# Kernel optimization log

Measured on AMD Instinct MI355X. Metric: run time of the kernel, lower is better.

Reference implementation:

```python
import jax, jax.numpy as jnp
import numpy as np

DIM = 1280
HEADS = 16
HEAD_DIM = DIM // HEADS  # 80
N_CHUNKS = 8
CHUNK = 1024
TOTAL = N_CHUNKS * CHUNK  # 8192 packed tokens


def rotate_half(x):
    x1, x2 = jnp.split(x, 2, axis=-1)
    return jnp.concatenate([-x2, x1], axis=-1)


def setup_inputs() -> dict:
    key = jax.random.key(0)
    k0, k1, k2 = jax.random.split(key, 3)
    hidden_states = jax.random.normal(k0, (TOTAL, DIM), dtype=jnp.float32)
    # 2D-rope style per-token angles, duplicated halves (standard vision RoPE layout)
    inv_freq = 1.0 / (10000.0 ** (jnp.arange(0, HEAD_DIM, 2, dtype=jnp.float32) / HEAD_DIM))
    pos = jnp.arange(TOTAL, dtype=jnp.float32)
    freqs = pos[:, None] * inv_freq[None, :]            # [T, HEAD_DIM//2]
    emb = jnp.concatenate([freqs, freqs], axis=-1)      # [T, HEAD_DIM]
    cos = jnp.cos(emb)
    sin = jnp.sin(emb)
    qkv_w = jax.random.normal(k1, (3 * DIM, DIM), dtype=jnp.float32) * 0.02
    qkv_b = jnp.zeros((3 * DIM,), dtype=jnp.float32)
    proj_w = jax.random.normal(k2, (DIM, DIM), dtype=jnp.float32) * 0.02
    proj_b = jnp.zeros((DIM,), dtype=jnp.float32)
    cu_seqlens = (jnp.arange(N_CHUNKS + 1, dtype=jnp.int32) * CHUNK)
    return {"hidden_states": hidden_states, "cos": cos, "sin": sin,
            "qkv_w": qkv_w, "qkv_b": qkv_b, "proj_w": proj_w, "proj_b": proj_b,
            "cu_seqlens": cu_seqlens}


def reference(hidden_states, cos, sin, qkv_w, qkv_b, proj_w, proj_b, cu_seqlens):
    # Equal-length chunks (cu_seqlens uniform): vectorize the Python chunk loop
    # as a leading batch axis n over chunks of length L.
    n = cu_seqlens.shape[0] - 1
    total, dim = hidden_states.shape
    L = total // n
    scaling = HEAD_DIM ** -0.5

    x = hidden_states.reshape(n, L, dim)
    qkv = x @ qkv_w.T + qkv_b                              # [n, L, 3*dim]
    qkv = qkv.reshape(n, L, 3, HEADS, HEAD_DIM)
    q, k, v = qkv[:, :, 0], qkv[:, :, 1], qkv[:, :, 2]     # [n, L, H, hd]

    # inline RoPE in fp32 (matches apply_rotary_pos_emb_vision)
    c = cos.reshape(n, L, 1, HEAD_DIM).astype(jnp.float32)
    s = sin.reshape(n, L, 1, HEAD_DIM).astype(jnp.float32)
    qf = q.astype(jnp.float32)
    kf = k.astype(jnp.float32)
    q = (qf * c + rotate_half(qf) * s).astype(q.dtype)
    k = (kf * c + rotate_half(kf) * s).astype(k.dtype)

    # naive per-chunk full attention: QK^T, fp32 softmax, PV
    scores = jnp.einsum('nlhd,nmhd->nhlm', q, k) * scaling  # [n, H, L, L]
    probs = jax.nn.softmax(scores.astype(jnp.float32), axis=-1).astype(q.dtype)
    out = jnp.einsum('nhlm,nmhd->nlhd', probs, v)           # [n, L, H, hd]
    out = out.reshape(n, L, dim)
    out = out @ proj_w.T + proj_b                           # [n, L, dim]
    return out.reshape(total, dim)
```

## Files before the change

### kernel.cpp

```cpp
#include <hip/hip_runtime.h>
#include <stdint.h>

#define DIM 1280
#define HEADS 16
#define HD 80
#define TOTAL 8192
#define CHUNK 1024
#define QKVN 3840

typedef __attribute__((ext_vector_type(8))) __bf16 bf16x8;
typedef __attribute__((ext_vector_type(4))) float floatx4;

typedef __attribute__((address_space(1))) const uint32_t gu32;
typedef __attribute__((address_space(3))) uint32_t lu32;

__device__ __forceinline__ void llds16(const void* g, void* l) {
  __builtin_amdgcn_global_load_lds((gu32*)g, (lu32*)l, 16, 0, 0);
}

__device__ __forceinline__ unsigned short f2b(float f) {
  union { __bf16 b; unsigned short u; } x; x.b = (__bf16)f; return x.u;
}
__device__ __forceinline__ float b2f(unsigned short u) {
  union { __bf16 b; unsigned short u; } x; x.u = u; return (float)x.b;
}
__device__ __forceinline__ float fexp2(float x) {
#if __has_builtin(__builtin_amdgcn_exp2f)
  return __builtin_amdgcn_exp2f(x);
#else
  return __expf(x * 0.6931471805599453f);
#endif
}

#define QSCALE (0.11180339887498949f * 1.44269504088896340f)

#define KT_SH (64 * 104)
#define VT_SH (80 * 72)

__global__ void cvt_bf16(const float* __restrict__ src, unsigned short* __restrict__ dst, int n4) {
  int i = blockIdx.x * 256 + threadIdx.x;
  if (i >= n4) return;
  float4 v = reinterpret_cast<const float4*>(src)[i];
  ushort4 o;
  o.x = f2b(v.x); o.y = f2b(v.y); o.z = f2b(v.z); o.w = f2b(v.w);
  reinterpret_cast<ushort4*>(dst)[i] = o;
}


__device__ __forceinline__ void stage_a64(const unsigned short* __restrict__ G,
                                          unsigned short* ls, int wv, int lane,
                                          int row0, int kk, int hi) {
#pragma unroll
  for (int t = 0; t < 2; ++t) {
    const int stripe = t * 8 + wv;
    const int rb = ((stripe >> 3) << 7) + ((stripe & 7) << 3) + hi;
    const int r = rb + (lane >> 3);
    const int ch = (lane & 7) ^ (r & 7);
    llds16(G + (size_t)(row0 + r) * DIM + kk + (ch << 3), ls + rb * 64);
  }
}

__device__ __forceinline__ void stage_b64(const unsigned short* __restrict__ G,
                                          unsigned short* ls, int wv, int lane,
                                          int row0, int kk, int hi) {
#pragma unroll
  for (int t = 0; t < 2; ++t) {
    const int stripe = t * 8 + wv;
    const int rb = ((stripe >> 2) << 6) + ((stripe & 3) << 3) + hi;
    const int r = rb + (lane >> 3);
    const int ch = (lane & 7) ^ (r & 7);
    llds16(G + (size_t)(row0 + r) * DIM + kk + (ch << 3), ls + rb * 64);
  }
}

__device__ __forceinline__ bf16x8 frg(const unsigned short* ls, int r, int cx) {
  return *reinterpret_cast<const bf16x8*>(ls + r * 64 + (cx << 3));
}

#define MFMA_BF16 __builtin_amdgcn_mfma_f32_16x16x32_bf16
#define LGKM0() asm volatile("s_waitcnt lgkmcnt(0)" ::: "memory")
#define BARR()  asm volatile("s_barrier" ::: "memory")

template<int MODE>
__launch_bounds__(512, 2)
__global__ void gemm8(const unsigned short* __restrict__ A,
                      const unsigned short* __restrict__ B,
                      const float* __restrict__ bias,
                      unsigned short* __restrict__ qo,
                      unsigned short* __restrict__ ko,
                      unsigned short* __restrict__ vo,
                      float* __restrict__ fo) {
  __shared__ __attribute__((aligned(16))) unsigned short lsA[2][256 * 64];
  __shared__ __attribute__((aligned(16))) unsigned short lsB[2][256 * 64];
  const int m0 = blockIdx.x * 256;
  const int n0 = blockIdx.y * 256;
  const int tid = threadIdx.x;
  const int wv = tid >> 6, lane = tid & 63;
  const int wr = wv >> 2, wc = wv & 3;
  const int q4 = lane >> 4, l15 = lane & 15;
  const int sx = l15 & 7;
  const int cx0 = q4 ^ sx;
  const int cx1 = (4 + q4) ^ sx;

  stage_a64(A, &lsA[0][0], wv, lane, m0, 0, 0);
  stage_b64(B, &lsB[0][0], wv, lane, n0, 0, 0);
  stage_b64(B, &lsB[0][0], wv, lane, n0, 0, 32);
  stage_a64(A, &lsA[0][0], wv, lane, m0, 0, 64);
  stage_b64(B, &lsB[1][0], wv, lane, n0, 64, 0);
  stage_a64(A, &lsA[1][0], wv, lane, m0, 64, 0);
  stage_b64(B, &lsB[1][0], wv, lane, n0, 64, 32);

  floatx4 acc[8][4];
#pragma unroll
  for (int i = 0; i < 8; ++i)
#pragma unroll
    for (int j = 0; j < 4; ++j)
      acc[i][j] = (floatx4){0.f, 0.f, 0.f, 0.f};

  asm volatile("s_waitcnt vmcnt(6)" ::: "memory");
  BARR();

  const int rA = wr * 128 + l15;
  const int rB = wc * 64 + l15;

  bf16x8 ArLo[4][2], ArHi[4][2], Blo[2][2], Bhi[2][2];

#pragma unroll 2
  for (int kt = 0; kt < 20; ++kt) {
    const unsigned short* la = &lsA[kt & 1][0];
    const unsigned short* lb = &lsB[kt & 1][0];
    unsigned short* aN = &lsA[(kt & 1) ^ 1][0];
    unsigned short* aC = &lsA[kt & 1][0];
    unsigned short* bC = &lsB[kt & 1][0];
    const bool st1 = (kt + 1 < 20);
    const bool st2 = (kt + 2 < 20);

    if (kt > 0) {
#pragma unroll
      for (int m = 0; m < 4; ++m)
#pragma unroll
        for (int n = 0; n < 2; ++n) {
          acc[m + 4][n] = MFMA_BF16(ArHi[m][0], Blo[n][0], acc[m + 4][n], 0, 0, 0);
          acc[m + 4][n] = MFMA_BF16(ArHi[m][1], Blo[n][1], acc[m + 4][n], 0, 0, 0);
        }
    }
#pragma unroll
    for (int m = 0; m < 4; ++m) {
      ArLo[m][0] = frg(la, rA + m * 16, cx0);
      ArLo[m][1] = frg(la, rA + m * 16, cx1);
    }
#pragma unroll
    for (int n = 0; n < 2; ++n) {
      Blo[n][0] = frg(lb, rB + n * 16, cx0);
      Blo[n][1] = frg(lb, rB + n * 16, cx1);
    }
    if (st1) stage_a64(A, aN, wv, lane, m0, (kt + 1) * 64, 64);
    LGKM0();
    BARR();

#pragma unroll
    for (int m = 0; m < 4; ++m)
#pragma unroll
      for (int n = 0; n < 2; ++n) {
        acc[m][n] = MFMA_BF16(ArLo[m][0], Blo[n][0], acc[m][n], 0, 0, 0);
        acc[m][n] = MFMA_BF16(ArLo[m][1], Blo[n][1], acc[m][n], 0, 0, 0);
      }
#pragma unroll
    for (int n = 0; n < 2; ++n) {
      Bhi[n][0] = frg(lb, rB + (n + 2) * 16, cx0);
      Bhi[n][1] = frg(lb, rB + (n + 2) * 16, cx1);
    }
    if (st2) stage_b64(B, bC, wv, lane, n0, (kt + 2) * 64, 0);
    LGKM0();
    BARR();

#pragma unroll
    for (int m = 0; m < 4; ++m)
#pragma unroll
      for (int n = 0; n < 2; ++n) {
        acc[m][n + 2] = MFMA_BF16(ArLo[m][0], Bhi[n][0], acc[m][n + 2], 0, 0, 0);
        acc[m][n + 2] = MFMA_BF16(ArLo[m][1], Bhi[n][1], acc[m][n + 2], 0, 0, 0);
      }
#pragma unroll
    for (int m = 0; m < 4; ++m) {
      ArHi[m][0] = frg(la, rA + (m + 4) * 16, cx0);
      ArHi[m][1] = frg(la, rA + (m + 4) * 16, cx1);
    }
    if (st2) stage_a64(A, aC, wv, lane, m0, (kt + 2) * 64, 0);
    LGKM0();
    BARR();

#pragma unroll
    for (int m = 0; m < 4; ++m)
#pragma unroll
      for (int n = 0; n < 2; ++n) {
        acc[m + 4][n + 2] = MFMA_BF16(ArHi[m][0], Bhi[n][0], acc[m + 4][n + 2], 0, 0, 0);
        acc[m + 4][n + 2] = MFMA_BF16(ArHi[m][1], Bhi[n][1], acc[m + 4][n + 2], 0, 0, 0);
      }
    if (st2) stage_b64(B, bC, wv, lane, n0, (kt + 2) * 64, 32);
    if (st2)      asm volatile("s_waitcnt vmcnt(6)" ::: "memory");
    else if (st1) asm volatile("s_waitcnt vmcnt(0)" ::: "memory");
    BARR();
  }

#pragma unroll
  for (int m = 0; m < 4; ++m)
#pragma unroll
    for (int n = 0; n < 2; ++n) {
      acc[m + 4][n] = MFMA_BF16(ArHi[m][0], Blo[n][0], acc[m + 4][n], 0, 0, 0);
      acc[m + 4][n] = MFMA_BF16(ArHi[m][1], Blo[n][1], acc[m + 4][n], 0, 0, 0);
    }

  if (MODE == 0) {
    if (blockIdx.y >= 10) {
      unsigned short* scr = (wv < 4) ? (&lsA[0][0] + wv * 8192)
                                     : (&lsB[0][0] + (wv - 4) * 8192);
      const int base_c = n0 - 2 * DIM + wc * 64;
#pragma unroll
      for (int n = 0; n < 4; ++n) {
        const int cloc = n * 16 + l15;
        const float bn = bias[2 * DIM + base_c + cloc];
        const int swz = (cloc & 7) << 4;
#pragma unroll
        for (int m = 0; m < 8; ++m) {
          const int rloc = m * 16 + q4 * 4;
          ushort4 w;
          w.x = f2b(acc[m][n][0] + bn);
          w.y = f2b(acc[m][n][1] + bn);
          w.z = f2b(acc[m][n][2] + bn);
          w.w = f2b(acc[m][n][3] + bn);
          *reinterpret_cast<ushort4*>(scr + cloc * 128 + (rloc ^ swz)) = w;
        }
      }
#pragma unroll
      for (int jtc = 0; jtc < 2; ++jtc) {
        const int rowg = m0 + wr * 128 + jtc * 64;
        const int chn = rowg >> 10, jtn = (rowg >> 6) & 15;
#pragma unroll
        for (int cb = 0; cb < 16; ++cb) {
          const int col = cb * 4 + q4;
          const int c = base_c + col;
          const int h = c / 80;
          const int d = c - h * 80;
          const int rloc = jtc * 64 + l15 * 4;
          const ushort4 w = *reinterpret_cast<const ushort4*>(
              scr + col * 128 + (rloc ^ ((col & 7) << 4)));
          *reinterpret_cast<ushort4*>(
              vo + (size_t)((chn * 16 + h) * 16 + jtn) * VT_SH + d * 72 + l15 * 4) = w;
        }
      }
      return;
    }
    unsigned short* os;
    int nloc = n0;
    if (blockIdx.y < 5) { os = qo; }
    else                { os = ko; nloc = n0 - DIM; }
#pragma unroll
    for (int n = 0; n < 4; ++n) {
      const int cg = wc * 64 + n * 16 + l15;
      const float bn = bias[n0 + cg];
#pragma unroll
      for (int m = 0; m < 8; ++m) {
#pragma unroll
        for (int r = 0; r < 4; ++r) {
          const int row = m0 + wr * 128 + m * 16 + q4 * 4 + r;
          os[(size_t)row * DIM + nloc + cg] = f2b(acc[m][n][r] + bn);
        }
      }
    }
    return;
  }
#pragma unroll
  for (int n = 0; n < 4; ++n) {
    const int cg = wc * 64 + n * 16 + l15;
    const float bn = bias[n0 + cg];
#pragma unroll
    for (int m = 0; m < 8; ++m) {
#pragma unroll
      for (int r = 0; r < 4; ++r) {
        const int row = m0 + wr * 128 + m * 16 + q4 * 4 + r;
        fo[(size_t)row * DIM + n0 + cg] = acc[m][n][r] + bn;
      }
    }
  }
}

__global__ void prep_k(const unsigned short* __restrict__ kbuf,
                       const float* __restrict__ cp, const float* __restrict__ sp,
                       unsigned short* __restrict__ kimg) {
  const int m = blockIdx.x, tid = threadIdx.x;
  const int ch = m >> 10, rl = m & 1023;
  const int jt = rl >> 6, rr = rl & 63;

  if (tid < 160) {
    const int h = tid / 10, j = tid - h * 10;
    const int d0 = 4 * j;
    const float4 c4 = *reinterpret_cast<const float4*>(cp + (size_t)m * HD + d0);
    const float4 s4 = *reinterpret_cast<const float4*>(sp + (size_t)m * HD + d0);
    const ushort4 lo = *reinterpret_cast<const ushort4*>(kbuf + (size_t)m * DIM + h * HD + d0);
    const ushort4 hi = *reinterpret_cast<const ushort4*>(kbuf + (size_t)m * DIM + h * HD + d0 + 40);
    ushort4 o1, o2;
    o1.x = f2b(b2f(lo.x) * c4.x - b2f(hi.x) * s4.x);
    o1.y = f2b(b2f(lo.y) * c4.y - b2f(hi.y) * s4.y);
    o1.z = f2b(b2f(lo.z) * c4.z - b2f(hi.z) * s4.z);
    o1.w = f2b(b2f(lo.w) * c4.w - b2f(hi.w) * s4.w);
    o2.x = f2b(b2f(hi.x) * c4.x + b2f(lo.x) * s4.x);
    o2.y = f2b(b2f(hi.y) * c4.y + b2f(lo.y) * s4.y);
    o2.z = f2b(b2f(hi.z) * c4.z + b2f(lo.z) * s4.z);
    o2.w = f2b(b2f(hi.w) * c4.w + b2f(lo.w) * s4.w);
    const size_t ob = ((size_t)((ch * 16 + h) * 16 + jt) * KT_SH) + rr * 104;
    *reinterpret_cast<ushort4*>(kimg + ob + d0) = o1;
    *reinterpret_cast<ushort4*>(kimg + ob + d0 + 40) = o2;
  } else {
    const int t = tid - 160;
    const int h = t / 6, qi = t - h * 6;
    const size_t ob = ((size_t)((ch * 16 + h) * 16 + jt) * KT_SH) + rr * 104;
    *reinterpret_cast<ushort4*>(kimg + ob + 80 + 4 * qi) = (ushort4){0, 0, 0, 0};
  }
}

__launch_bounds__(256, 2)
__global__ void attn_k(const unsigned short* __restrict__ qbuf,
                       const unsigned short* __restrict__ kimg,
                       const unsigned short* __restrict__ vimg,
                       const float* __restrict__ cp, const float* __restrict__ sp,
                       unsigned short* __restrict__ ob) {
  __shared__ __attribute__((aligned(16))) unsigned short lsK[2][KT_SH];
  __shared__ __attribute__((aligned(16))) unsigned short lsV[2][VT_SH];
  __shared__ __attribute__((aligned(16))) unsigned short lsP[128 * 72];

  const int bx = blockIdx.x;
  const int qt = bx & 7, h = (bx >> 3) & 15, ch = bx >> 7;
  const int tid = threadIdx.x, wv = tid >> 6, lane = tid & 63;
  const int q4 = lane >> 4, l15 = lane & 15;
  const int qrow_loc = qt * 128 + wv * 32;

  bf16x8 aq[2][3];
#pragma unroll
  for (int mt = 0; mt < 2; ++mt) {
    const int m_row = ch * 1024 + qrow_loc + mt * 16 + l15;
    const unsigned short* qr = qbuf + (size_t)m_row * DIM + h * HD;
    const float* cr = cp + (size_t)m_row * HD;
    const float* sr = sp + (size_t)m_row * HD;
#pragma unroll
    for (int ks = 0; ks < 3; ++ks) {
      const int d0 = ks * 32 + q4 * 8;
      union { ushort4 u4[2]; bf16x8 v; } out;
      if (d0 < 80) {
        const bool hi = (d0 >= 40);
        const int pd = hi ? d0 - 40 : d0 + 40;
        const float sg = hi ? 1.0f : -1.0f;
        const ushort4 xa = *reinterpret_cast<const ushort4*>(qr + d0);
        const ushort4 xc = *reinterpret_cast<const ushort4*>(qr + d0 + 4);
        const ushort4 pa = *reinterpret_cast<const ushort4*>(qr + pd);
        const ushort4 pc = *reinterpret_cast<const ushort4*>(qr + pd + 4);
        const float4 c0 = *reinterpret_cast<const float4*>(cr + d0);
        const float4 c1 = *reinterpret_cast<const float4*>(cr + d0 + 4);
        const float4 s0 = *reinterpret_cast<const float4*>(sr + d0);
        const float4 s1 = *reinterpret_cast<const float4*>(sr + d0 + 4);
        ushort4 o0, o1;
        o0.x = f2b((b2f(xa.x) * c0.x + sg * b2f(pa.x) * s0.x) * QSCALE);
        o0.y = f2b((b2f(xa.y) * c0.y + sg * b2f(pa.y) * s0.y) * QSCALE);
        o0.z = f2b((b2f(xa.z) * c0.z + sg * b2f(pa.z) * s0.z) * QSCALE);
        o0.w = f2b((b2f(xa.w) * c0.w + sg * b2f(pa.w) * s0.w) * QSCALE);
        o1.x = f2b((b2f(xc.x) * c1.x + sg * b2f(pc.x) * s1.x) * QSCALE);
        o1.y = f2b((b2f(xc.y) * c1.y + sg * b2f(pc.y) * s1.y) * QSCALE);
        o1.z = f2b((b2f(xc.z) * c1.z + sg * b2f(pc.z) * s1.z) * QSCALE);
        o1.w = f2b((b2f(xc.w) * c1.w + sg * b2f(pc.w) * s1.w) * QSCALE);
        out.u4[0] = o0; out.u4[1] = o1;
      } else {
        out.u4[0] = (ushort4){0, 0, 0, 0};
        out.u4[1] = (ushort4){0, 0, 0, 0};
      }
      aq[mt][ks] = out.v;
    }
  }

  floatx4 oacc[2][5];
  float lpart[2] = {0.f, 0.f};
#pragma unroll
  for (int mt = 0; mt < 2; ++mt)
#pragma unroll
    for (int t = 0; t < 5; ++t) oacc[mt][t] = (floatx4){0.f, 0.f, 0.f, 0.f};

  const char* kbase = (const char*)(kimg + (size_t)(ch * 16 + h) * 16 * KT_SH);
  const char* vbase = (const char*)(vimg + (size_t)(ch * 16 + h) * 16 * VT_SH);

  auto stage_kv = [&](int jt, char* lk, char* lv) {
    const char* kg = kbase + (size_t)jt * (KT_SH * 2);
#pragma unroll
    for (int r = 0; r < 4; ++r) {
      const int off = (r * 4 + wv) * 1024;
      if (off < KT_SH * 2)
        llds16(kg + off + lane * 16, lk + off);
    }
    const char* vg = vbase + (size_t)jt * (VT_SH * 2);
#pragma unroll
    for (int r = 0; r < 3; ++r) {
      const int off = (r * 4 + wv) * 1024;
      if (off < VT_SH * 2) {
        if (off + 1024 <= VT_SH * 2) llds16(vg + off + lane * 16, lv + off);
        else if (lane < 16)          llds16(vg + off + lane * 16, lv + off);
      }
    }
  };

  stage_kv(0, (char*)lsK[0], (char*)lsV[0]);

  for (int jt = 0; jt < 16; ++jt) {
    const int cur = jt & 1;
    __syncthreads();
    if (jt + 1 < 16)
      stage_kv(jt + 1, (char*)lsK[cur ^ 1], (char*)lsV[cur ^ 1]);

    const unsigned short* lk = lsK[cur];
    const unsigned short* lv = lsV[cur];

    floatx4 sfr[2][4];
    __builtin_amdgcn_s_setprio(1);
#pragma unroll
    for (int c = 0; c < 4; ++c) {
      const bf16x8 ak0 = *reinterpret_cast<const bf16x8*>(&lk[(c * 16 + l15) * 104 + 0  + q4 * 8]);
      const bf16x8 ak1 = *reinterpret_cast<const bf16x8*>(&lk[(c * 16 + l15) * 104 + 32 + q4 * 8]);
      const bf16x8 ak2 = *reinterpret_cast<const bf16x8*>(&lk[(c * 16 + l15) * 104 + 64 + q4 * 8]);
#pragma unroll
      for (int mt = 0; mt < 2; ++mt) {
        floatx4 s = (floatx4){0.f, 0.f, 0.f, 0.f};
        s = __builtin_amdgcn_mfma_f32_16x16x32_bf16(ak0, aq[mt][0], s, 0, 0, 0);
        s = __builtin_amdgcn_mfma_f32_16x16x32_bf16(ak1, aq[mt][1], s, 0, 0, 0);
        s = __builtin_amdgcn_mfma_f32_16x16x32_bf16(ak2, aq[mt][2], s, 0, 0, 0);
        sfr[mt][c] = s;
      }
    }
    __builtin_amdgcn_s_setprio(0);

#pragma unroll
    for (int mt = 0; mt < 2; ++mt)
#pragma unroll
      for (int c = 0; c < 4; ++c) {
        const float p0 = fexp2(sfr[mt][c][0]);
        const float p1 = fexp2(sfr[mt][c][1]);
        const float p2 = fexp2(sfr[mt][c][2]);
        const float p3 = fexp2(sfr[mt][c][3]);
        lpart[mt] += (p0 + p1) + (p2 + p3);
        ushort4 w;
        w.x = f2b(p0); w.y = f2b(p1); w.z = f2b(p2); w.w = f2b(p3);
        *reinterpret_cast<ushort4*>(&lsP[(wv * 32 + mt * 16 + l15) * 72 + c * 16 + q4 * 4]) = w;
      }

    __builtin_amdgcn_s_setprio(1);
#pragma unroll
    for (int ks = 0; ks < 2; ++ks) {
      const bf16x8 ap0 = *reinterpret_cast<const bf16x8*>(&lsP[(wv * 32 + 0  + l15) * 72 + ks * 32 + q4 * 8]);
      const bf16x8 ap1 = *reinterpret_cast<const bf16x8*>(&lsP[(wv * 32 + 16 + l15) * 72 + ks * 32 + q4 * 8]);
#pragma unroll
      for (int t = 0; t < 5; ++t) {
        const bf16x8 bv = *reinterpret_cast<const bf16x8*>(&lv[(t * 16 + l15) * 72 + ks * 32 + q4 * 8]);
        oacc[0][t] = __builtin_amdgcn_mfma_f32_16x16x32_bf16(ap0, bv, oacc[0][t], 0, 0, 0);
        oacc[1][t] = __builtin_amdgcn_mfma_f32_16x16x32_bf16(ap1, bv, oacc[1][t], 0, 0, 0);
      }
    }
    __builtin_amdgcn_s_setprio(0);
  }

#pragma unroll
  for (int mt = 0; mt < 2; ++mt) {
    lpart[mt] += __shfl_xor(lpart[mt], 16, 64);
    lpart[mt] += __shfl_xor(lpart[mt], 32, 64);
  }
  float inv[2];
  inv[0] = 1.0f / lpart[0];
  inv[1] = 1.0f / lpart[1];

  float invr[2][4];
#pragma unroll
  for (int mt = 0; mt < 2; ++mt)
#pragma unroll
    for (int r = 0; r < 4; ++r)
      invr[mt][r] = __shfl(inv[mt], q4 * 4 + r, 64);

#pragma unroll
  for (int mt = 0; mt < 2; ++mt)
#pragma unroll
    for (int t = 0; t < 5; ++t)
#pragma unroll
      for (int r = 0; r < 4; ++r) {
        const int gr = ch * CHUNK + qrow_loc + mt * 16 + q4 * 4 + r;
        const int gc = h * HD + t * 16 + l15;
        ob[(size_t)gr * DIM + gc] = f2b(oacc[mt][t][r] * invr[mt][r]);
      }
}

extern "C" void kernel_launch(void* const* d_in, const int* in_sizes, int n_in,
                              void* d_out, int out_size, void* d_ws, size_t ws_size,
                              hipStream_t stream) {
  (void)in_sizes; (void)n_in; (void)out_size; (void)ws_size;
  const float* hs    = (const float*)d_in[0];
  const float* cosp  = (const float*)d_in[1];
  const float* sinp  = (const float*)d_in[2];
  const float* qkvw  = (const float*)d_in[3];
  const float* qkvb  = (const float*)d_in[4];
  const float* projw = (const float*)d_in[5];
  const float* projb = (const float*)d_in[6];

  char* ws = (char*)d_ws;
  unsigned short* xb   = (unsigned short*)(ws + 0);
  unsigned short* wq   = (unsigned short*)(ws + 20971520);
  unsigned short* qbuf = (unsigned short*)(ws + 30801920);
  unsigned short* kbuf = (unsigned short*)(ws + 51773440);
  unsigned short* vimg = (unsigned short*)(ws + 72744960);
  unsigned short* wp   = (unsigned short*)(ws + 96337920);
  unsigned short* kimg = (unsigned short*)(ws + 99614720);
  unsigned short* obuf = xb;

  cvt_bf16<<<TOTAL * DIM / 4 / 256, 256, 0, stream>>>(hs, xb, TOTAL * DIM / 4);
  cvt_bf16<<<QKVN * DIM / 4 / 256, 256, 0, stream>>>(qkvw, wq, QKVN * DIM / 4);
  cvt_bf16<<<DIM * DIM / 4 / 256, 256, 0, stream>>>(projw, wp, DIM * DIM / 4);

  gemm8<0><<<dim3(TOTAL / 256, QKVN / 256), 512, 0, stream>>>(
      xb, wq, qkvb, qbuf, kbuf, vimg, nullptr);

  prep_k<<<TOTAL, 256, 0, stream>>>(kbuf, cosp, sinp, kimg);

  attn_k<<<1024, 256, 0, stream>>>(qbuf, kimg, vimg, cosp, sinp, obuf);

  gemm8<1><<<dim3(TOTAL / 256, DIM / 256), 512, 0, stream>>>(
      obuf, wp, projb, nullptr, nullptr, nullptr, (float*)d_out);
}
```

Before: 334.8 us.

## Keep softmax probabilities in registers by permuting K rows, drop P LDS buffer

Prep_k now writes K rows in a permuted order inside each 64-row tile, so the QK^T MFMA output fragments land in exactly the layout needed as the A operand of the PV MFMA. The P tile therefore stays in registers instead of being written to and read back from shared memory, which removes the lsP buffer and its LDS traffic. Freeing that shared memory lets occupancy rise from 2 to 3 blocks per CU via the launch bounds. The risk is register pressure under the tighter launch bound, which could cause spills, and the permutation must exactly match the MFMA lane mapping for the result to stay correct.

New measurement: 329.8 us. No clear change (-1.5%).

```diff
diff --git a/kernel.cpp b/kernel.cpp
--- a/kernel.cpp
+++ b/kernel.cpp
@@ -291,6 +291,8 @@
   const int m = blockIdx.x, tid = threadIdx.x;
   const int ch = m >> 10, rl = m & 1023;
   const int jt = rl >> 6, rr = rl & 63;
+  const int rrp = ((((rr >> 2) & 1) * 2 + (rr >> 5)) << 4) |
+                  (((rr >> 3) & 3) << 2) | (rr & 3);
 
   if (tid < 160) {
     const int h = tid / 10, j = tid - h * 10;
@@ -308,18 +310,18 @@
     o2.y = f2b(b2f(hi.y) * c4.y + b2f(lo.y) * s4.y);
     o2.z = f2b(b2f(hi.z) * c4.z + b2f(lo.z) * s4.z);
     o2.w = f2b(b2f(hi.w) * c4.w + b2f(lo.w) * s4.w);
-    const size_t ob = ((size_t)((ch * 16 + h) * 16 + jt) * KT_SH) + rr * 104;
+    const size_t ob = ((size_t)((ch * 16 + h) * 16 + jt) * KT_SH) + rrp * 104;
     *reinterpret_cast<ushort4*>(kimg + ob + d0) = o1;
     *reinterpret_cast<ushort4*>(kimg + ob + d0 + 40) = o2;
   } else {
     const int t = tid - 160;
     const int h = t / 6, qi = t - h * 6;
-    const size_t ob = ((size_t)((ch * 16 + h) * 16 + jt) * KT_SH) + rr * 104;
+    const size_t ob = ((size_t)((ch * 16 + h) * 16 + jt) * KT_SH) + rrp * 104;
     *reinterpret_cast<ushort4*>(kimg + ob + 80 + 4 * qi) = (ushort4){0, 0, 0, 0};
   }
 }
 
-__launch_bounds__(256, 2)
+__launch_bounds__(256, 3)
 __global__ void attn_k(const unsigned short* __restrict__ qbuf,
                        const unsigned short* __restrict__ kimg,
                        const unsigned short* __restrict__ vimg,
@@ -327,7 +329,6 @@
                        unsigned short* __restrict__ ob) {
   __shared__ __attribute__((aligned(16))) unsigned short lsK[2][KT_SH];
   __shared__ __attribute__((aligned(16))) unsigned short lsV[2][VT_SH];
-  __shared__ __attribute__((aligned(16))) unsigned short lsP[128 * 72];
 
   const int bx = blockIdx.x;
   const int qt = bx & 7, h = (bx >> 3) & 15, ch = bx >> 7;
@@ -352,21 +353,21 @@
         const float sg = hi ? 1.0f : -1.0f;
         const ushort4 xa = *reinterpret_cast<const ushort4*>(qr + d0);
         const ushort4 xc = *reinterpret_cast<const ushort4*>(qr + d0 + 4);
-        const ushort4 pa = *reinterpret_cast<const ushort4*>(qr + pd);
-        const ushort4 pc = *reinterpret_cast<const ushort4*>(qr + pd + 4);
+        const ushort4 pa_ = *reinterpret_cast<const ushort4*>(qr + pd);
+        const ushort4 pc_ = *reinterpret_cast<const ushort4*>(qr + pd + 4);
         const float4 c0 = *reinterpret_cast<const float4*>(cr + d0);
         const float4 c1 = *reinterpret_cast<const float4*>(cr + d0 + 4);
         const float4 s0 = *reinterpret_cast<const float4*>(sr + d0);
         const float4 s1 = *reinterpret_cast<const float4*>(sr + d0 + 4);
         ushort4 o0, o1;
-        o0.x = f2b((b2f(xa.x) * c0.x + sg * b2f(pa.x) * s0.x) * QSCALE);
-        o0.y = f2b((b2f(xa.y) * c0.y + sg * b2f(pa.y) * s0.y) * QSCALE);
-        o0.z = f2b((b2f(xa.z) * c0.z + sg * b2f(pa.z) * s0.z) * QSCALE);
-        o0.w = f2b((b2f(xa.w) * c0.w + sg * b2f(pa.w) * s0.w) * QSCALE);
-        o1.x = f2b((b2f(xc.x) * c1.x + sg * b2f(pc.x) * s1.x) * QSCALE);
-        o1.y = f2b((b2f(xc.y) * c1.y + sg * b2f(pc.y) * s1.y) * QSCALE);
-        o1.z = f2b((b2f(xc.z) * c1.z + sg * b2f(pc.z) * s1.z) * QSCALE);
-        o1.w = f2b((b2f(xc.w) * c1.w + sg * b2f(pc.w) * s1.w) * QSCALE);
+        o0.x = f2b((b2f(xa.x) * c0.x + sg * b2f(pa_.x) * s0.x) * QSCALE);
+        o0.y = f2b((b2f(xa.y) * c0.y + sg * b2f(pa_.y) * s0.y) * QSCALE);
+        o0.z = f2b((b2f(xa.z) * c0.z + sg * b2f(pa_.z) * s0.z) * QSCALE);
+        o0.w = f2b((b2f(xa.w) * c0.w + sg * b2f(pa_.w) * s0.w) * QSCALE);
+        o1.x = f2b((b2f(xc.x) * c1.x + sg * b2f(pc_.x) * s1.x) * QSCALE);
+        o1.y = f2b((b2f(xc.y) * c1.y + sg * b2f(pc_.y) * s1.y) * QSCALE);
+        o1.z = f2b((b2f(xc.z) * c1.z + sg * b2f(pc_.z) * s1.z) * QSCALE);
+        o1.w = f2b((b2f(xc.w) * c1.w + sg * b2f(pc_.w) * s1.w) * QSCALE);
         out.u4[0] = o0; out.u4[1] = o1;
       } else {
         out.u4[0] = (ushort4){0, 0, 0, 0};
@@ -434,6 +435,8 @@
     }
     __builtin_amdgcn_s_setprio(0);
 
+    union Pk { unsigned short u[8]; bf16x8 v; };
+    Pk pa[2][2];
 #pragma unroll
     for (int mt = 0; mt < 2; ++mt)
 #pragma unroll
@@ -443,16 +446,18 @@
         const float p2 = fexp2(sfr[mt][c][2]);
         const float p3 = fexp2(sfr[mt][c][3]);
         lpart[mt] += (p0 + p1) + (p2 + p3);
-        ushort4 w;
-        w.x = f2b(p0); w.y = f2b(p1); w.z = f2b(p2); w.w = f2b(p3);
-        *reinterpret_cast<ushort4*>(&lsP[(wv * 32 + mt * 16 + l15) * 72 + c * 16 + q4 * 4]) = w;
+        const int ks = c & 1, jb = (c >> 1) << 2;
+        pa[mt][ks].u[jb + 0] = f2b(p0);
+        pa[mt][ks].u[jb + 1] = f2b(p1);
+        pa[mt][ks].u[jb + 2] = f2b(p2);
+        pa[mt][ks].u[jb + 3] = f2b(p3);
       }
 
     __builtin_amdgcn_s_setprio(1);
 #pragma unroll
     for (int ks = 0; ks < 2; ++ks) {
-      const bf16x8 ap0 = *reinterpret_cast<const bf16x8*>(&lsP[(wv * 32 + 0  + l15) * 72 + ks * 32 + q4 * 8]);
-      const bf16x8 ap1 = *reinterpret_cast<const bf16x8*>(&lsP[(wv * 32 + 16 + l15) * 72 + ks * 32 + q4 * 8]);
+      const bf16x8 ap0 = pa[0][ks].v;
+      const bf16x8 ap1 = pa[1][ks].v;
 #pragma unroll
       for (int t = 0; t < 5; ++t) {
         const bf16x8 bv = *reinterpret_cast<const bf16x8*>(&lv[(t * 16 + l15) * 72 + ks * 32 + q4 * 8]);
```
